# Kernel tuning notes

Hardware: AMD Instinct MI355X
Metric: run time of the kernel (lower is better)

## Reference

```python
import jax, jax.numpy as jnp
import numpy as np

HIDDEN = 2560
NUM_HEADS = 32
HEAD_DIM = HIDDEN // NUM_HEADS          # 80
ROTARY_DIM = int(0.4 * HEAD_DIM)        # 32 (partial rotary)
ROPE_BASE = 10000.0
SCALE = HEAD_DIM ** -0.5


def _apply_partial_rope(x, pos):
    # x: [B, S, H, D], pos: [B, S] int. NeoX-style rotation on first ROTARY_DIM dims.
    half = ROTARY_DIM // 2
    inv_freq = 1.0 / (ROPE_BASE ** (jnp.arange(half, dtype=jnp.float32) / half))
    ang = pos.astype(jnp.float32)[..., None] * inv_freq      # [B, S, half]
    cos = jnp.cos(ang)[:, :, None, :]                        # [B, S, 1, half]
    sin = jnp.sin(ang)[:, :, None, :]
    x1 = x[..., :half]
    x2 = x[..., half:ROTARY_DIM]
    x_pass = x[..., ROTARY_DIM:]
    o1 = x1 * cos - x2 * sin
    o2 = x2 * cos + x1 * sin
    return jnp.concatenate([o1, o2, x_pass], axis=-1)


def setup_inputs() -> dict:
    key = jax.random.key(0)
    ks = jax.random.split(key, 5)
    B, S = 2, 2048
    hidden_states = jax.random.normal(ks[0], (B, S, HIDDEN), dtype=jnp.float32)
    position_ids = jnp.tile(jnp.arange(S, dtype=jnp.int32)[None, :], (B, 1))
    w_std = HIDDEN ** -0.5
    Wqkv = jax.random.normal(ks[1], (HIDDEN, 3 * HIDDEN), dtype=jnp.float32) * w_std
    bqkv = jax.random.normal(ks[2], (3 * HIDDEN,), dtype=jnp.float32) * 0.02
    Wd = jax.random.normal(ks[3], (HIDDEN, HIDDEN), dtype=jnp.float32) * w_std
    bd = jax.random.normal(ks[4], (HIDDEN,), dtype=jnp.float32) * 0.02
    return {"position_ids": position_ids, "hidden_states": hidden_states,
            "Wqkv": Wqkv, "bqkv": bqkv, "Wd": Wd, "bd": bd}


def reference(position_ids, hidden_states, Wqkv, bqkv, Wd, bd):
    B, S, _ = hidden_states.shape
    qkv = hidden_states @ Wqkv + bqkv                         # [B, S, 3*HIDDEN]
    q, k, v = jnp.split(qkv, 3, axis=-1)
    q = q.reshape(B, S, NUM_HEADS, HEAD_DIM)
    k = k.reshape(B, S, NUM_HEADS, HEAD_DIM)
    v = v.reshape(B, S, NUM_HEADS, HEAD_DIM)
    q = _apply_partial_rope(q, position_ids)
    k = _apply_partial_rope(k, position_ids)
    # causal self-attention (RadixAttention prefill with empty prefix)
    scores = jnp.einsum('bqhd,bkhd->bhqk', q, k) * SCALE      # [B, H, S, S]
    causal = jnp.tril(jnp.ones((S, S), dtype=bool))
    scores = jnp.where(causal[None, None], scores, jnp.finfo(scores.dtype).min)
    probs = jax.nn.softmax(scores, axis=-1)
    attn = jnp.einsum('bhqk,bkhd->bqhd', probs, v).reshape(B, S, HIDDEN)
    return attn @ Wd + bd
```

## Files before the change

### kernel.cpp

```cpp
#include <hip/hip_runtime.h>

#define HIDDEN 2560
#define NHEADS 32
#define HDIM 80
#define DPAD 96
#define SEQ 2048
#define M_TOK 4096
#define N_QKV 7680
#define ATT_SCALE 0.11180339887498949f

typedef __attribute__((ext_vector_type(4))) float f32x4;
typedef __attribute__((ext_vector_type(16))) float f32x16;
typedef __attribute__((ext_vector_type(4))) int i32x4;
typedef __attribute__((ext_vector_type(8))) short bf16x8;
typedef __attribute__((ext_vector_type(8))) unsigned short ushort8;

#define BAR() asm volatile("s_barrier" ::: "memory")

__device__ __forceinline__ unsigned short f2bf(float f) {
    unsigned int u = __float_as_uint(f);
    u += 0x7FFFu + ((u >> 16) & 1u);
    return (unsigned short)(u >> 16);
}
__device__ __forceinline__ float bf2f(unsigned short h) {
    return __uint_as_float(((unsigned int)h) << 16);
}

__device__ __forceinline__ void async_copy16(unsigned short* lds, const unsigned short* g) {
    __builtin_amdgcn_global_load_lds((const __attribute__((address_space(1))) void*)g,
                                     (__attribute__((address_space(3))) void*)lds, 16, 0, 0);
}

__device__ __forceinline__ int cvt_pk_bf16(float lo, float hi) {
    int d;
    asm("v_cvt_pk_bf16_f32 %0, %1, %2" : "=v"(d) : "v"(lo), "v"(hi));
    return d;
}

__global__ __launch_bounds__(256) void cvt_kernel(const float* __restrict__ in,
                                                  unsigned short* __restrict__ out, int n8) {
    int i = blockIdx.x * 256 + threadIdx.x;
    if (i >= n8) return;
    const float4* p = (const float4*)in + (size_t)i * 2;
    float4 a = p[0], b = p[1];
    ushort8 o;
    o[0] = f2bf(a.x); o[1] = f2bf(a.y); o[2] = f2bf(a.z); o[3] = f2bf(a.w);
    o[4] = f2bf(b.x); o[5] = f2bf(b.y); o[6] = f2bf(b.z); o[7] = f2bf(b.w);
    *((ushort8*)out + i) = o;
}

__global__ __launch_bounds__(256) void transpose_kernel(const float* __restrict__ in,
                                                        unsigned short* __restrict__ out,
                                                        int R, int C) {
    __shared__ unsigned short tile[64][66];
    const int r0 = blockIdx.y * 64, c0 = blockIdx.x * 64;
    const int t = threadIdx.x;
#pragma unroll
    for (int rep = 0; rep < 16; ++rep) {
        int idx = rep * 256 + t;
        int i = idx >> 6, j = idx & 63;
        tile[i][j] = f2bf(in[(size_t)(r0 + i) * C + (c0 + j)]);
    }
    __syncthreads();
#pragma unroll
    for (int rep = 0; rep < 16; ++rep) {
        int idx = rep * 256 + t;
        int j = idx >> 6, i = idx & 63;
        out[(size_t)(c0 + j) * R + (r0 + i)] = tile[i][j];
    }
}

template <int OUT_BF16>
__global__ __launch_bounds__(1024, 4) void gemm256(const unsigned short* __restrict__ A,
                                                   const unsigned short* __restrict__ Bt,
                                                   const float* __restrict__ bias,
                                                   void* __restrict__ C,
                                                   int M, int N, int K) {
    __shared__ __align__(16) unsigned short S[4][16384];
    const int t = threadIdx.x;
    const int lane = t & 63, wid = t >> 6;
    const int wm = wid >> 2, wn = wid & 3;
    const int l15 = lane & 15, lhi = lane >> 4;

    const int cpx = (int)gridDim.x >> 3;
    const int wg = ((int)blockIdx.x % 8) * cpx + ((int)blockIdx.x >> 3);
    const int bm = (wg & 15) * 256;
    const int bn = (wg >> 4) * 256;

    const int srow = t >> 2;
    const int scol = ((t & 3) ^ ((srow >> 1) & 3)) * 8;
    const unsigned short* Abase = A + (size_t)bm * K;
    const unsigned short* Bbase = Bt + (size_t)bn * K;
    const int NP = K >> 5;

    int aoff[4], boff[4];
#pragma unroll
    for (int i = 0; i < 4; ++i) {
        int r = wm * 64 + i * 16 + l15;
        aoff[i] = r * 32 + ((lhi ^ ((r >> 1) & 3)) * 8);
    }
#pragma unroll
    for (int f = 0; f < 4; ++f) {
        int r = wn * 64 + f * 16 + l15;
        boff[f] = 8192 + r * 32 + ((lhi ^ ((r >> 1) & 3)) * 8);
    }

    f32x4 acc[4][4] = {};

#define STAGE_A(J) { const int j_ = (J);                                               \
    async_copy16(&S[j_ & 3][0] + t * 8,                                                \
                 Abase + (size_t)srow * K + j_ * 32 + scol); }
#define STAGE_B(J) { const int j_ = (J);                                               \
    async_copy16(&S[j_ & 3][8192] + t * 8,                                             \
                 Bbase + (size_t)srow * K + j_ * 32 + scol); }

#define PERIOD(J, VM, DOSTAGE) {                                                       \
    const int jp_ = (J);                                                               \
    asm volatile("s_waitcnt vmcnt(" #VM ")" ::: "memory");                             \
    BAR();                                                                             \
    const unsigned short* sl = &S[jp_ & 3][0];                                         \
    if (DOSTAGE) STAGE_A(jp_ + 3);                                                     \
    bf16x8 bq[4], afr[2];                                                              \
    _Pragma("unroll")                                                                  \
    for (int f = 0; f < 4; ++f) bq[f] = *(const bf16x8*)(sl + boff[f]);                \
    afr[0] = *(const bf16x8*)(sl + aoff[0]);                                           \
    afr[1] = *(const bf16x8*)(sl + aoff[1]);                                           \
    __builtin_amdgcn_s_setprio(1);                                                     \
    _Pragma("unroll")                                                                  \
    for (int i = 0; i < 2; ++i)                                                        \
        _Pragma("unroll")                                                              \
        for (int f = 0; f < 4; ++f)                                                    \
            acc[i][f] = __builtin_amdgcn_mfma_f32_16x16x32_bf16(afr[i], bq[f],         \
                                                                acc[i][f], 0, 0, 0);   \
    __builtin_amdgcn_s_setprio(0);                                                     \
    if (DOSTAGE) STAGE_B(jp_ + 3);                                                     \
    afr[0] = *(const bf16x8*)(sl + aoff[2]);                                           \
    afr[1] = *(const bf16x8*)(sl + aoff[3]);                                           \
    __builtin_amdgcn_s_setprio(1);                                                     \
    _Pragma("unroll")                                                                  \
    for (int i = 0; i < 2; ++i)                                                        \
        _Pragma("unroll")                                                              \
        for (int f = 0; f < 4; ++f)                                                    \
            acc[2 + i][f] = __builtin_amdgcn_mfma_f32_16x16x32_bf16(afr[i], bq[f],     \
                                                                    acc[2 + i][f],     \
                                                                    0, 0, 0);          \
    __builtin_amdgcn_s_setprio(0); }

    STAGE_A(0); STAGE_B(0);
    STAGE_A(1); STAGE_B(1);
    STAGE_A(2); STAGE_B(2);

    for (int p = 0; p < NP - 3; ++p) {
        PERIOD(p, 4, 1);
    }
    PERIOD(NP - 3, 4, 0);
    PERIOD(NP - 2, 2, 0);
    PERIOD(NP - 1, 0, 0);

#undef PERIOD
#undef STAGE_A
#undef STAGE_B

#pragma unroll
    for (int f = 0; f < 4; ++f) {
        const int col = bn + wn * 64 + f * 16 + l15;
        const float bv = bias[col];
#pragma unroll
        for (int i = 0; i < 4; ++i) {
            const int row0 = bm + wm * 64 + i * 16 + lhi * 4;
#pragma unroll
            for (int r = 0; r < 4; ++r) {
                float v = acc[i][f][r] + bv;
                if (OUT_BF16)
                    ((unsigned short*)C)[(size_t)(row0 + r) * N + col] = f2bf(v);
                else
                    ((float*)C)[(size_t)(row0 + r) * N + col] = v;
            }
        }
    }
}

__global__ __launch_bounds__(256) void pack_rope_kernel(const unsigned short* __restrict__ qkv,
                                                        const int* __restrict__ pos_ids,
                                                        unsigned short* __restrict__ Qb,
                                                        unsigned short* __restrict__ Kb,
                                                        unsigned short* __restrict__ Vt) {
    int g = blockIdx.x * 256 + threadIdx.x;
    int s = g & (SEQ - 1);
    int bh = g >> 11;
    int b = bh >> 5;
    int h = bh & 31;
    int m = b * SEQ + s;
    const unsigned short* base = qkv + (size_t)m * N_QKV + h * HDIM;
    unsigned short* Qrow = Qb + ((size_t)bh * SEQ + s) * DPAD;
    unsigned short* Krow = Kb + ((size_t)bh * SEQ + s) * DPAD;
    unsigned short* Vcol = Vt + (size_t)bh * HDIM * SEQ + s;

    float pos = (float)pos_ids[m];
    float qv[32], kv[32];
#pragma unroll
    for (int c = 0; c < 4; ++c) {
        ushort8 qc = *(const ushort8*)(base + c * 8);
        ushort8 kc = *(const ushort8*)(base + HIDDEN + c * 8);
#pragma unroll
        for (int j = 0; j < 8; ++j) {
            qv[c * 8 + j] = bf2f(qc[j]);
            kv[c * 8 + j] = bf2f(kc[j]);
        }
    }
#pragma unroll
    for (int d = 0; d < 16; ++d) {
        float inv = __expf(-(float)d * 0.5756462732485115f);
        float ang = pos * inv;
        float sn, cs;
        __sincosf(ang, &sn, &cs);
        float qcs = cs * ATT_SCALE, qsn = sn * ATT_SCALE;
        float x1 = qv[d], x2 = qv[d + 16];
        qv[d] = x1 * qcs - x2 * qsn;
        qv[d + 16] = x2 * qcs + x1 * qsn;
        x1 = kv[d]; x2 = kv[d + 16];
        kv[d] = x1 * cs - x2 * sn;
        kv[d + 16] = x2 * cs + x1 * sn;
    }
#pragma unroll
    for (int c = 0; c < 4; ++c) {
        ushort8 qo, ko;
#pragma unroll
        for (int j = 0; j < 8; ++j) {
            qo[j] = f2bf(qv[c * 8 + j]);
            ko[j] = f2bf(kv[c * 8 + j]);
        }
        *(ushort8*)(Qrow + c * 8) = qo;
        *(ushort8*)(Krow + c * 8) = ko;
    }
#pragma unroll
    for (int c = 4; c < 10; ++c) {
        ushort8 qc = *(const ushort8*)(base + c * 8);
        ushort8 qo;
#pragma unroll
        for (int j = 0; j < 8; ++j) qo[j] = f2bf(bf2f(qc[j]) * ATT_SCALE);
        *(ushort8*)(Qrow + c * 8) = qo;
        *(ushort8*)(Krow + c * 8) = *(const ushort8*)(base + HIDDEN + c * 8);
    }
#pragma unroll
    for (int d = 0; d < HDIM; ++d) Vcol[(size_t)d * SEQ] = base[2 * HIDDEN + d];
}

__global__ __launch_bounds__(512) void flash_kernel(const unsigned short* __restrict__ Qb,
                                                    const unsigned short* __restrict__ Kb,
                                                    const unsigned short* __restrict__ Vt,
                                                    unsigned short* __restrict__ attn) {
    __shared__ __align__(16) unsigned short Klds[64 * 128];
    __shared__ __align__(16) unsigned short Vlds[96 * 64];

    const int bh = blockIdx.x;
    const int qb = 7 - (int)blockIdx.y;
    const int q0b = qb * 256;
    const int nkt = 4 * qb + 4;
    const int t = threadIdx.x;
    const int lane = t & 63, wid = t >> 6;
    const int l31 = lane & 31, h = lane >> 5, l7 = lane & 7;
    const int q0w = q0b + wid * 32;
    const int swz = l7 << 3;

    const unsigned short* Kbase = Kb + (size_t)bh * SEQ * DPAD;
    const unsigned short* Vbase = Vt + (size_t)bh * HDIM * SEQ;

    bf16x8 qf[5];
    {
        const unsigned short* Qrow = Qb + ((size_t)bh * SEQ + q0w + l31) * DPAD + h * 8;
#pragma unroll
        for (int dc = 0; dc < 5; ++dc) qf[dc] = *(const bf16x8*)(Qrow + dc * 16);
    }

    ((int*)Vlds)[2560 + t] = 0;

    f32x16 acc0 = {}, acc1 = {}, acc2 = {};
    float mrow = -1e30f, lrow = 0.f;

    const int kidx1 = 512 + t;
    const int kr0 = t / 10, kc0 = t % 10;
    const int kr1 = kidx1 / 10, kc1 = kidx1 % 10;
    const int vr0 = t >> 3, vc0 = t & 7;
    const int vr1 = (512 + t) >> 3, vc1 = t & 7;
    const int kd0 = kr0 * 128 + ((kc0 * 8) ^ ((kr0 & 7) << 3));
    const int kd1 = kr1 * 128 + ((kc1 * 8) ^ ((kr1 & 7) << 3));
    const int vd0 = vr0 * 64 + ((vc0 * 8) ^ ((vr0 & 7) << 3));
    const int vd1 = vr1 * 64 + ((vc1 * 8) ^ ((vr1 & 7) << 3));

    ushort8 kreg0, kreg1, vreg0, vreg1;
    kreg0 = *(const ushort8*)(Kbase + (size_t)kr0 * DPAD + kc0 * 8);
    if (t < 128) kreg1 = *(const ushort8*)(Kbase + (size_t)kr1 * DPAD + kc1 * 8);
    vreg0 = *(const ushort8*)(Vbase + (size_t)vr0 * SEQ + vc0 * 8);
    if (t < 128) vreg1 = *(const ushort8*)(Vbase + (size_t)vr1 * SEQ + vc1 * 8);

    for (int kt = 0; kt < nkt; ++kt) {
        const int k0 = kt * 64;
        __syncthreads();
        *(ushort8*)(Klds + kd0) = kreg0;
        if (t < 128) *(ushort8*)(Klds + kd1) = kreg1;
        *(ushort8*)(Vlds + vd0) = vreg0;
        if (t < 128) *(ushort8*)(Vlds + vd1) = vreg1;
        __syncthreads();
        if (kt + 1 < nkt) {
            const int kn = k0 + 64;
            kreg0 = *(const ushort8*)(Kbase + (size_t)(kn + kr0) * DPAD + kc0 * 8);
            if (t < 128) kreg1 = *(const ushort8*)(Kbase + (size_t)(kn + kr1) * DPAD + kc1 * 8);
            vreg0 = *(const ushort8*)(Vbase + (size_t)vr0 * SEQ + kn + vc0 * 8);
            if (t < 128) vreg1 = *(const ushort8*)(Vbase + (size_t)vr1 * SEQ + kn + vc1 * 8);
        }
        if (k0 > q0w + 31) continue;

        f32x16 s0 = {}, s1 = {};
        __builtin_amdgcn_s_setprio(1);
#pragma unroll
        for (int dc = 0; dc < 5; ++dc) {
            const int co = (dc * 16 + h * 8) ^ swz;
            bf16x8 ka = *(const bf16x8*)(Klds + l31 * 128 + co);
            bf16x8 kb2 = *(const bf16x8*)(Klds + (32 + l31) * 128 + co);
            s0 = __builtin_amdgcn_mfma_f32_32x32x16_bf16(ka, qf[dc], s0, 0, 0, 0);
            s1 = __builtin_amdgcn_mfma_f32_32x32x16_bf16(kb2, qf[dc], s1, 0, 0, 0);
        }
        __builtin_amdgcn_s_setprio(0);

        const int qg = q0w + l31;
        if (k0 + 63 > q0w) {
#pragma unroll
            for (int r = 0; r < 16; ++r) {
                const int kg = k0 + (r & 3) + 8 * (r >> 2) + 4 * h;
                if (kg > qg) s0[r] = -2e30f;
                if (kg + 32 > qg) s1[r] = -2e30f;
            }
        }
        float pmax = s0[0];
#pragma unroll
        for (int r = 1; r < 16; ++r) pmax = fmaxf(pmax, s0[r]);
#pragma unroll
        for (int r = 0; r < 16; ++r) pmax = fmaxf(pmax, s1[r]);
        pmax = fmaxf(pmax, __shfl_xor(pmax, 32, 64));
        if (!__all(pmax <= mrow + 8.0f)) {
            float mnew = fmaxf(mrow, pmax);
            float scl = __expf(mrow - mnew);
            mrow = mnew;
            lrow *= scl;
#pragma unroll
            for (int r = 0; r < 16; ++r) {
                float sq = __shfl(scl, (r & 3) + 8 * (r >> 2) + 4 * h, 64);
                acc0[r] *= sq; acc1[r] *= sq; acc2[r] *= sq;
            }
        }
        float ps = 0.f;
#pragma unroll
        for (int r = 0; r < 16; ++r) { s0[r] = __expf(s0[r] - mrow); ps += s0[r]; }
#pragma unroll
        for (int r = 0; r < 16; ++r) { s1[r] = __expf(s1[r] - mrow); ps += s1[r]; }
        lrow += ps + __shfl_xor(ps, 32, 64);
        i32x4 af[2][2];
#pragma unroll
        for (int ks = 0; ks < 2; ++ks) {
            const f32x16& sv = ks ? s1 : s0;
            int pk0[2], pk1[2], pk2[2], pk3[2];
#pragma unroll
            for (int i = 0; i < 2; ++i) {
                pk0[i] = cvt_pk_bf16(sv[2 * i], sv[2 * i + 1]);
                pk1[i] = cvt_pk_bf16(sv[4 + 2 * i], sv[5 + 2 * i]);
                pk2[i] = cvt_pk_bf16(sv[8 + 2 * i], sv[9 + 2 * i]);
                pk3[i] = cvt_pk_bf16(sv[12 + 2 * i], sv[13 + 2 * i]);
            }
#pragma unroll
            for (int i = 0; i < 2; ++i) {
                const int o0 = __shfl_xor(pk0[i], 32, 64);
                const int o1 = __shfl_xor(pk1[i], 32, 64);
                af[ks][0][i]     = h ? o1     : pk0[i];
                af[ks][0][2 + i] = h ? pk1[i] : o0;
                const int o2 = __shfl_xor(pk2[i], 32, 64);
                const int o3 = __shfl_xor(pk3[i], 32, 64);
                af[ks][1][i]     = h ? o3     : pk2[i];
                af[ks][1][2 + i] = h ? pk3[i] : o2;
            }
        }
        __builtin_amdgcn_s_setprio(1);
#pragma unroll
        for (int ds = 0; ds < 3; ++ds) {
            f32x16& ac = ds == 0 ? acc0 : (ds == 1 ? acc1 : acc2);
            const int vrow = (ds * 32 + l31) * 64;
#pragma unroll
            for (int ks = 0; ks < 2; ++ks)
#pragma unroll
                for (int kh = 0; kh < 2; ++kh) {
                    bf16x8 vb = *(const bf16x8*)(Vlds + vrow + ((ks * 32 + kh * 16 + h * 8) ^ swz));
                    bf16x8 pa = __builtin_bit_cast(bf16x8, af[ks][kh]);
                    ac = __builtin_amdgcn_mfma_f32_32x32x16_bf16(pa, vb, ac, 0, 0, 0);
                }
        }
        __builtin_amdgcn_s_setprio(0);
    }

    const int hh = bh & 31, b = bh >> 5;
    const float linv = 1.0f / lrow;
#pragma unroll
    for (int r = 0; r < 16; ++r) {
        const int ql = (r & 3) + 8 * (r >> 2) + 4 * h;
        const float lv = __shfl(linv, ql, 64);
        const int row = b * SEQ + q0b + wid * 32 + ql;
        unsigned short* orow = attn + (size_t)row * HIDDEN + hh * HDIM;
        orow[l31] = f2bf(acc0[r] * lv);
        orow[32 + l31] = f2bf(acc1[r] * lv);
        if (l31 < 16) orow[64 + l31] = f2bf(acc2[r] * lv);
    }
}

extern "C" void kernel_launch(void* const* d_in, const int* in_sizes, int n_in,
                              void* d_out, int out_size, void* d_ws, size_t ws_size,
                              hipStream_t stream) {
    const int* pos = (const int*)d_in[0];
    const float* hid = (const float*)d_in[1];
    const float* Wqkv = (const float*)d_in[2];
    const float* bqkv = (const float*)d_in[3];
    const float* Wd = (const float*)d_in[4];
    const float* bd = (const float*)d_in[5];
    float* out = (float*)d_out;
    char* ws = (char*)d_ws;

    unsigned short* WqkvT = (unsigned short*)(ws);
    unsigned short* WdT   = (unsigned short*)(ws + 39321600);
    unsigned short* Xbf   = (unsigned short*)(ws + 52428800);
    unsigned short* qkv   = (unsigned short*)(ws + 73400320);
    unsigned short* Qbuf  = (unsigned short*)(ws + 136314880);
    unsigned short* Kbuf  = (unsigned short*)(ws + 161480704);
    unsigned short* Vt    = (unsigned short*)(ws + 186646528);
    unsigned short* attnb = Xbf;

    cvt_kernel<<<(M_TOK * HIDDEN / 8 + 255) / 256, 256, 0, stream>>>(hid, Xbf, M_TOK * HIDDEN / 8);
    transpose_kernel<<<dim3(N_QKV / 64, HIDDEN / 64), 256, 0, stream>>>(Wqkv, WqkvT, HIDDEN, N_QKV);
    transpose_kernel<<<dim3(HIDDEN / 64, HIDDEN / 64), 256, 0, stream>>>(Wd, WdT, HIDDEN, HIDDEN);
    gemm256<1><<<(M_TOK / 256) * (N_QKV / 256), 1024, 0, stream>>>(Xbf, WqkvT, bqkv, qkv,
                                                                   M_TOK, N_QKV, HIDDEN);
    pack_rope_kernel<<<(64 * SEQ) / 256, 256, 0, stream>>>(qkv, pos, Qbuf, Kbuf, Vt);
    flash_kernel<<<dim3(64, 8), 512, 0, stream>>>(Qbuf, Kbuf, Vt, attnb);
    gemm256<0><<<(M_TOK / 256) * (HIDDEN / 256), 1024, 0, stream>>>(attnb, WdT, bd, out,
                                                                    M_TOK, HIDDEN, HIDDEN);
}
```

Before: 380.4 us.

## Shrink GEMM block tile to 128x256 with 512 threads and triple buffering

The shared GEMM kernel now uses a 128x256 output tile per block with 8 waves instead of 256x256 with 16 waves. Its LDS pipeline drops from four stages to three, with the A and B loads issued together per stage. The aim is more blocks (better CU fill for the smaller output projection GEMM) and less LDS per block, at the cost of lower data reuse per block and a shallower prefetch pipeline.

Measured after the change: 416.9 us. 9.6% more time.

```diff
diff --git a/kernel.cpp b/kernel.cpp
--- a/kernel.cpp
+++ b/kernel.cpp
@@ -71,24 +71,32 @@
 }
 
 template <int OUT_BF16>
-__global__ __launch_bounds__(1024, 4) void gemm256(const unsigned short* __restrict__ A,
-                                                   const unsigned short* __restrict__ Bt,
-                                                   const float* __restrict__ bias,
-                                                   void* __restrict__ C,
-                                                   int M, int N, int K) {
-    __shared__ __align__(16) unsigned short S[4][16384];
+__global__ __launch_bounds__(512, 4) void gemm256(const unsigned short* __restrict__ A,
+                                                  const unsigned short* __restrict__ Bt,
+                                                  const float* __restrict__ bias,
+                                                  void* __restrict__ C,
+                                                  int M, int N, int K) {
+    __shared__ __align__(16) unsigned short S[3][12288];
     const int t = threadIdx.x;
     const int lane = t & 63, wid = t >> 6;
     const int wm = wid >> 2, wn = wid & 3;
     const int l15 = lane & 15, lhi = lane >> 4;
 
+    const int nmt = M >> 7;
     const int cpx = (int)gridDim.x >> 3;
     const int wg = ((int)blockIdx.x % 8) * cpx + ((int)blockIdx.x >> 3);
-    const int bm = (wg & 15) * 256;
-    const int bn = (wg >> 4) * 256;
-
-    const int srow = t >> 2;
-    const int scol = ((t & 3) ^ ((srow >> 1) & 3)) * 8;
+    const int bm = (wg % nmt) * 128;
+    const int bn = (wg / nmt) * 256;
+
+    const int arow_s = t >> 2;
+    const int acol_s = ((t & 3) ^ ((arow_s >> 1) & 3)) * 8;
+    int brow_s[2], bcol_s[2];
+#pragma unroll
+    for (int c = 0; c < 2; ++c) {
+        int idx = t + c * 512;
+        brow_s[c] = idx >> 2;
+        bcol_s[c] = ((idx & 3) ^ ((brow_s[c] >> 1) & 3)) * 8;
+    }
     const unsigned short* Abase = A + (size_t)bm * K;
     const unsigned short* Bbase = Bt + (size_t)bn * K;
     const int NP = K >> 5;
@@ -102,24 +110,24 @@
 #pragma unroll
     for (int f = 0; f < 4; ++f) {
         int r = wn * 64 + f * 16 + l15;
-        boff[f] = 8192 + r * 32 + ((lhi ^ ((r >> 1) & 3)) * 8);
+        boff[f] = 4096 + r * 32 + ((lhi ^ ((r >> 1) & 3)) * 8);
     }
 
     f32x4 acc[4][4] = {};
 
-#define STAGE_A(J) { const int j_ = (J);                                               \
-    async_copy16(&S[j_ & 3][0] + t * 8,                                                \
-                 Abase + (size_t)srow * K + j_ * 32 + scol); }
-#define STAGE_B(J) { const int j_ = (J);                                               \
-    async_copy16(&S[j_ & 3][8192] + t * 8,                                             \
-                 Bbase + (size_t)srow * K + j_ * 32 + scol); }
+#define STAGE(J) { const int j_ = (J); unsigned short* d = &S[j_ % 3][0];              \
+    async_copy16(d + t * 8, Abase + (size_t)arow_s * K + j_ * 32 + acol_s);            \
+    _Pragma("unroll")                                                                  \
+    for (int c = 0; c < 2; ++c)                                                        \
+        async_copy16(d + 4096 + (t + c * 512) * 8,                                     \
+                     Bbase + (size_t)brow_s[c] * K + j_ * 32 + bcol_s[c]); }
 
 #define PERIOD(J, VM, DOSTAGE) {                                                       \
     const int jp_ = (J);                                                               \
     asm volatile("s_waitcnt vmcnt(" #VM ")" ::: "memory");                             \
     BAR();                                                                             \
-    const unsigned short* sl = &S[jp_ & 3][0];                                         \
-    if (DOSTAGE) STAGE_A(jp_ + 3);                                                     \
+    const unsigned short* sl = &S[jp_ % 3][0];                                         \
+    if (DOSTAGE) STAGE(jp_ + 2);                                                       \
     bf16x8 bq[4], afr[2];                                                              \
     _Pragma("unroll")                                                                  \
     for (int f = 0; f < 4; ++f) bq[f] = *(const bf16x8*)(sl + boff[f]);                \
@@ -133,7 +141,6 @@
             acc[i][f] = __builtin_amdgcn_mfma_f32_16x16x32_bf16(afr[i], bq[f],         \
                                                                 acc[i][f], 0, 0, 0);   \
     __builtin_amdgcn_s_setprio(0);                                                     \
-    if (DOSTAGE) STAGE_B(jp_ + 3);                                                     \
     afr[0] = *(const bf16x8*)(sl + aoff[2]);                                           \
     afr[1] = *(const bf16x8*)(sl + aoff[3]);                                           \
     __builtin_amdgcn_s_setprio(1);                                                     \
@@ -146,20 +153,17 @@
                                                                     0, 0, 0);          \
     __builtin_amdgcn_s_setprio(0); }
 
-    STAGE_A(0); STAGE_B(0);
-    STAGE_A(1); STAGE_B(1);
-    STAGE_A(2); STAGE_B(2);
-
-    for (int p = 0; p < NP - 3; ++p) {
-        PERIOD(p, 4, 1);
-    }
-    PERIOD(NP - 3, 4, 0);
-    PERIOD(NP - 2, 2, 0);
+    STAGE(0);
+    STAGE(1);
+
+    for (int p = 0; p < NP - 2; ++p) {
+        PERIOD(p, 3, 1);
+    }
+    PERIOD(NP - 2, 3, 0);
     PERIOD(NP - 1, 0, 0);
 
 #undef PERIOD
-#undef STAGE_A
-#undef STAGE_B
+#undef STAGE
 
 #pragma unroll
     for (int f = 0; f < 4; ++f) {
@@ -434,10 +438,10 @@
     cvt_kernel<<<(M_TOK * HIDDEN / 8 + 255) / 256, 256, 0, stream>>>(hid, Xbf, M_TOK * HIDDEN / 8);
     transpose_kernel<<<dim3(N_QKV / 64, HIDDEN / 64), 256, 0, stream>>>(Wqkv, WqkvT, HIDDEN, N_QKV);
     transpose_kernel<<<dim3(HIDDEN / 64, HIDDEN / 64), 256, 0, stream>>>(Wd, WdT, HIDDEN, HIDDEN);
-    gemm256<1><<<(M_TOK / 256) * (N_QKV / 256), 1024, 0, stream>>>(Xbf, WqkvT, bqkv, qkv,
-                                                                   M_TOK, N_QKV, HIDDEN);
+    gemm256<1><<<(M_TOK / 128) * (N_QKV / 256), 512, 0, stream>>>(Xbf, WqkvT, bqkv, qkv,
+                                                                  M_TOK, N_QKV, HIDDEN);
     pack_rope_kernel<<<(64 * SEQ) / 256, 256, 0, stream>>>(qkv, pos, Qbuf, Kbuf, Vt);
     flash_kernel<<<dim3(64, 8), 512, 0, stream>>>(Qbuf, Kbuf, Vt, attnb);
-    gemm256<0><<<(M_TOK / 256) * (HIDDEN / 256), 1024, 0, stream>>>(attnb, WdT, bd, out,
-                                                                    M_TOK, HIDDEN, HIDDEN);
-}
+    gemm256<0><<<(M_TOK / 128) * (HIDDEN / 256), 512, 0, stream>>>(attnb, WdT, bd, out,
+                                                                   M_TOK, HIDDEN, HIDDEN);
+}
```

## Use 256x160 tiled GEMM for output projection to fill all CUs

Applied to the files above, without the earlier changes.

Replaces the 256x256-tile GEMM for the attention output projection with a new 256x160-tile kernel, so the grid has 256 blocks instead of 160 and matches the CU count. The new kernel uses a 4-stage async-copy LDS pipeline with 32-wide K steps and XOR-swizzled shared memory. Smaller tiles lower arithmetic intensity per block, and some threads issue redundant B loads.

Measured after the change: 376.7 us, median of 3. No clear change (-1.0%).

```diff
diff --git a/kernel.cpp b/kernel.cpp
--- a/kernel.cpp
+++ b/kernel.cpp
@@ -180,6 +180,102 @@
     }
 }
 
+__global__ __launch_bounds__(1024, 4) void gemm160(const unsigned short* __restrict__ A,
+                                                   const unsigned short* __restrict__ Bt,
+                                                   const float* __restrict__ bias,
+                                                   float* __restrict__ C,
+                                                   int M, int N, int K) {
+    __shared__ __align__(16) unsigned short S[4][13312];
+    const int t = threadIdx.x;
+    const int lane = t & 63, wid = t >> 6;
+    const int wm = wid >> 1, wn = wid & 1;
+    const int l15 = lane & 15, lhi = lane >> 4;
+
+    const int cpx = (int)gridDim.x >> 3;
+    const int wg = ((int)blockIdx.x % 8) * cpx + ((int)blockIdx.x >> 3);
+    const int bm = (wg & 15) * 256;
+    const int bn = (wg >> 4) * 160;
+
+    const int srow = t >> 2;
+    const int scol = ((t & 3) ^ ((srow >> 1) & 3)) * 8;
+    const int bidx = (t < 640) ? t : (t - 640);
+    const int brow = bidx >> 2;
+    const int bcol = ((bidx & 3) ^ ((brow >> 1) & 3)) * 8;
+    const unsigned short* Abase = A + (size_t)bm * K;
+    const unsigned short* Bbase = Bt + (size_t)bn * K;
+    const int NP = K >> 5;
+
+    int aoff[2], boff[5];
+#pragma unroll
+    for (int i = 0; i < 2; ++i) {
+        int r = wm * 32 + i * 16 + l15;
+        aoff[i] = r * 32 + ((lhi ^ ((r >> 1) & 3)) * 8);
+    }
+#pragma unroll
+    for (int f = 0; f < 5; ++f) {
+        int r = wn * 80 + f * 16 + l15;
+        boff[f] = 8192 + r * 32 + ((lhi ^ ((r >> 1) & 3)) * 8);
+    }
+
+    f32x4 acc[2][5] = {};
+
+#define STAGE_A(J) { const int j_ = (J);                                               \
+    async_copy16(&S[j_ & 3][0] + t * 8,                                                \
+                 Abase + (size_t)srow * K + j_ * 32 + scol); }
+#define STAGE_B(J) { const int j_ = (J);                                               \
+    async_copy16(&S[j_ & 3][8192] + bidx * 8,                                          \
+                 Bbase + (size_t)brow * K + j_ * 32 + bcol); }
+
+#define PERIOD(J, VM, DOSTAGE) {                                                       \
+    const int jp_ = (J);                                                               \
+    asm volatile("s_waitcnt vmcnt(" #VM ")" ::: "memory");                             \
+    BAR();                                                                             \
+    const unsigned short* sl = &S[jp_ & 3][0];                                         \
+    if (DOSTAGE) STAGE_A(jp_ + 3);                                                     \
+    bf16x8 bq[5], afr[2];                                                              \
+    _Pragma("unroll")                                                                  \
+    for (int f = 0; f < 5; ++f) bq[f] = *(const bf16x8*)(sl + boff[f]);                \
+    afr[0] = *(const bf16x8*)(sl + aoff[0]);                                           \
+    afr[1] = *(const bf16x8*)(sl + aoff[1]);                                           \
+    if (DOSTAGE) STAGE_B(jp_ + 3);                                                     \
+    __builtin_amdgcn_s_setprio(1);                                                     \
+    _Pragma("unroll")                                                                  \
+    for (int i = 0; i < 2; ++i)                                                        \
+        _Pragma("unroll")                                                              \
+        for (int f = 0; f < 5; ++f)                                                    \
+            acc[i][f] = __builtin_amdgcn_mfma_f32_16x16x32_bf16(afr[i], bq[f],         \
+                                                                acc[i][f], 0, 0, 0);   \
+    __builtin_amdgcn_s_setprio(0); }
+
+    STAGE_A(0); STAGE_B(0);
+    STAGE_A(1); STAGE_B(1);
+    STAGE_A(2); STAGE_B(2);
+
+    for (int p = 0; p < NP - 3; ++p) {
+        PERIOD(p, 4, 1);
+    }
+    PERIOD(NP - 3, 4, 0);
+    PERIOD(NP - 2, 2, 0);
+    PERIOD(NP - 1, 0, 0);
+
+#undef PERIOD
+#undef STAGE_A
+#undef STAGE_B
+
+#pragma unroll
+    for (int f = 0; f < 5; ++f) {
+        const int col = bn + wn * 80 + f * 16 + l15;
+        const float bv = bias[col];
+#pragma unroll
+        for (int i = 0; i < 2; ++i) {
+            const int row0 = bm + wm * 32 + i * 16 + lhi * 4;
+#pragma unroll
+            for (int r = 0; r < 4; ++r)
+                C[(size_t)(row0 + r) * N + col] = acc[i][f][r] + bv;
+        }
+    }
+}
+
 __global__ __launch_bounds__(256) void pack_rope_kernel(const unsigned short* __restrict__ qkv,
                                                         const int* __restrict__ pos_ids,
                                                         unsigned short* __restrict__ Qb,
@@ -438,6 +534,6 @@
                                                                    M_TOK, N_QKV, HIDDEN);
     pack_rope_kernel<<<(64 * SEQ) / 256, 256, 0, stream>>>(qkv, pos, Qbuf, Kbuf, Vt);
     flash_kernel<<<dim3(64, 8), 512, 0, stream>>>(Qbuf, Kbuf, Vt, attnb);
-    gemm256<0><<<(M_TOK / 256) * (HIDDEN / 256), 1024, 0, stream>>>(attnb, WdT, bd, out,
-                                                                    M_TOK, HIDDEN, HIDDEN);
-}
+    gemm160<<<(M_TOK / 256) * (HIDDEN / 160), 1024, 0, stream>>>(attnb, WdT, bd, out,
+                                                                 M_TOK, HIDDEN, HIDDEN);
+}
```
